# Kernel tuning notes

Hardware: AMD Instinct MI355X
Metric: run time of the kernel (lower is better)

The kernel has to match this reference:

```python
import jax, jax.numpy as jnp
import numpy as np

B, H, S, D = 2, 12, 3456, 32
FEATS_PER_T = 216
WINDOW_LEN = 8
ACT_SIZE = 16
IMG_FEAT_SIZE = 196
DECODER_ONLY = False


def eye_mask(seq_len, feats_per_t, window_len, act_size, img_feat_size, decoder_only=False):
    """Boolean [S, S] mask replicating get_eye_block_mask's memory_mask."""
    idx = jnp.arange(seq_len)
    q_t = (idx // feats_per_t)[:, None]          # [S,1]
    kv_t = (idx // feats_per_t)[None, :]         # [1,S]
    q_m = (idx % feats_per_t)[:, None]
    kv_m = (idx % feats_per_t)[None, :]
    proprio_idx_mod = 2 + 1 + 1
    img_start = feats_per_t - img_feat_size
    joint_start = img_start - act_size

    causal = (q_t >= kv_t) & (q_t - kv_t < window_len)
    is_q_img = q_m >= img_start
    is_kv_img = kv_m >= img_start
    is_q_joint = (q_m >= joint_start) & (q_m < img_start)
    is_kv_joint = (kv_m >= joint_start) & (kv_m < img_start)
    is_kv_proprio = kv_m == proprio_idx_mod

    img_to_img = ~(is_q_img & is_kv_img)
    same_t = q_t == kv_t
    joint_past_joint = ~(is_q_joint & is_kv_joint & ~same_t)
    proprio_past = ~(is_kv_proprio & (kv_t < q_t))
    past_image = ~(is_kv_img & (kv_t < q_t))
    m = causal & img_to_img & joint_past_joint & proprio_past & past_image
    if decoder_only:
        m = m & ~(is_q_img & ~is_kv_img)
    return m


def setup_inputs() -> dict:
    key = jax.random.key(0)
    kq, kk, kv = jax.random.split(key, 3)
    return {
        "q": jax.random.normal(kq, (B, H, S, D), dtype=jnp.float32),
        "k": jax.random.normal(kk, (B, H, S, D), dtype=jnp.float32),
        "v": jax.random.normal(kv, (B, H, S, D), dtype=jnp.float32),
        "feats_per_t": FEATS_PER_T,
        "window_len": WINDOW_LEN,
        "act_size": ACT_SIZE,
        "img_feat_size": IMG_FEAT_SIZE,
    }


def reference(q, k, v, feats_per_t, window_len, act_size, img_feat_size):
    seq_len = q.shape[2]
    mask = eye_mask(seq_len, feats_per_t, window_len, act_size,
                    img_feat_size, DECODER_ONLY)  # [S,S]
    scale = 1.0 / jnp.sqrt(jnp.array(q.shape[-1], q.dtype))
    scores = jnp.einsum("bhqd,bhkd->bhqk", q, k) * scale
    neg = jnp.asarray(jnp.finfo(scores.dtype).min, scores.dtype)
    scores = jnp.where(mask[None, None], scores, neg)
    attn = jax.nn.softmax(scores, axis=-1)
    return jnp.einsum("bhqk,bhkd->bhqd", attn, v)
```

## Files before the change

kernel.cpp:

```cpp
#include <hip/hip_runtime.h>

#define SEQ   3456
#define DH    32
#define FPT   216
#define NT    16
#define IMG0  20
#define SCALE 0.17677669529663687f

#define KPAD 40
#define VPAD 168
#define PPAD 36

typedef __attribute__((ext_vector_type(8))) short bf16x8;
typedef __attribute__((ext_vector_type(4))) float f32x4;

#define MFMA16(a,b,c) __builtin_amdgcn_mfma_f32_16x16x32_bf16(a,b,c,0,0,0)

__device__ __forceinline__ unsigned short bfh(float f) {
    unsigned u = __float_as_uint(f);
    u += 0x7FFFu + ((u >> 16) & 1u);
    return (unsigned short)(u >> 16);
}
__device__ __forceinline__ float bff(unsigned short h) {
    return __uint_as_float((unsigned)h << 16);
}
__device__ __forceinline__ void split8(const float* f, bf16x8& hi, bf16x8& lo) {
    #pragma unroll
    for (int j = 0; j < 8; ++j) {
        unsigned short h = bfh(f[j]);
        hi[j] = (short)h;
        lo[j] = (short)bfh(f[j] - bff(h));
    }
}

__global__ __launch_bounds__(256)
void eye_attn_mfma(const float* __restrict__ q, const float* __restrict__ k,
                   const float* __restrict__ v, float* __restrict__ out) {
    __shared__ __align__(16) unsigned short KsHi[160 * KPAD];
    __shared__ __align__(16) unsigned short KsLo[160 * KPAD];
    __shared__ __align__(16) unsigned short VtHi[DH * VPAD];
    __shared__ __align__(16) unsigned short VtLo[DH * VPAD];
    __shared__ __align__(16) float Pl[4 * 16 * PPAD];

    const int t = blockIdx.x, bh = blockIdx.y, tid = threadIdx.x;
    const size_t base = (size_t)bh * SEQ * DH;
    const int dmax = (t < 7) ? t : 7;
    const int nkeys = IMG0 * (dmax + 1);

    for (int i = tid; i < 160 * 8; i += 256) {
        const int g = i >> 3, c = i & 7;
        float4 kk = make_float4(0.f,0.f,0.f,0.f), vv = make_float4(0.f,0.f,0.f,0.f);
        if (g < nkeys) {
            const int d = g / IMG0, jj = g - d * IMG0;
            const size_t row = base + (size_t)((t - d) * FPT + jj) * DH + c * 4;
            kk = *(const float4*)(k + row);
            vv = *(const float4*)(v + row);
        }
        const float kf[4] = {kk.x, kk.y, kk.z, kk.w};
        const float vf[4] = {vv.x, vv.y, vv.z, vv.w};
        ushort4 khi, klo;
        unsigned short* ah = (unsigned short*)&khi;
        unsigned short* al = (unsigned short*)&klo;
        #pragma unroll
        for (int e = 0; e < 4; ++e) {
            const unsigned short h = bfh(kf[e]);
            ah[e] = h;
            al[e] = bfh(kf[e] - bff(h));
        }
        *(ushort4*)(KsHi + g * KPAD + c * 4) = khi;
        *(ushort4*)(KsLo + g * KPAD + c * 4) = klo;
        #pragma unroll
        for (int e = 0; e < 4; ++e) {
            const unsigned short h = bfh(vf[e]);
            VtHi[(c * 4 + e) * VPAD + g] = h;
            VtLo[(c * 4 + e) * VPAD + g] = bfh(vf[e] - bff(h));
        }
    }
    __syncthreads();

    const int wv = tid >> 6, lane = tid & 63;
    const int col = lane & 15, quad = lane >> 4;

    int mtiles[4]; int mcnt;
    if (wv == 0)      { mtiles[0]=0;  mtiles[1]=2;  mtiles[2]=3;  mtiles[3]=0; mcnt=3; }
    else if (wv == 1) { mtiles[0]=1;  mtiles[1]=4;  mtiles[2]=5;  mtiles[3]=0; mcnt=3; }
    else if (wv == 2) { mtiles[0]=6;  mtiles[1]=7;  mtiles[2]=8;  mtiles[3]=9; mcnt=4; }
    else              { mtiles[0]=10; mtiles[1]=11; mtiles[2]=12; mtiles[3]=13; mcnt=4; }

    bf16x8 bones;
    #pragma unroll
    for (int j = 0; j < 8; ++j) bones[j] = (short)(col == 0 ? 0x3F80 : 0);

    float* myP = Pl + wv * 16 * PPAD;
    const int nkt = (nkeys + 31) >> 5;

    for (int mi = 0; mi < mcnt; ++mi) {
        const int mb = mtiles[mi] * 16;
        bf16x8 qhi, qlo;
        {
            const int qc = min(mb + col, FPT - 1);
            const float* qp = q + base + (size_t)(t * FPT + qc) * DH + quad * 8;
            float qf[8];
            const float4 a0 = *(const float4*)qp;
            const float4 a1 = *(const float4*)(qp + 4);
            qf[0]=a0.x*SCALE; qf[1]=a0.y*SCALE; qf[2]=a0.z*SCALE; qf[3]=a0.w*SCALE;
            qf[4]=a1.x*SCALE; qf[5]=a1.y*SCALE; qf[6]=a1.z*SCALE; qf[7]=a1.w*SCALE;
            split8(qf, qhi, qlo);
        }
        f32x4 oacc0 = {0.f,0.f,0.f,0.f}, oacc1 = {0.f,0.f,0.f,0.f};
        f32x4 lacc = {0.f,0.f,0.f,0.f};

        for (int kt = 0; kt < nkt; ++kt) {
            f32x4 s[2];
            #pragma unroll
            for (int h = 0; h < 2; ++h) {
                const int key = kt * 32 + h * 16 + col;
                const bf16x8 bhi = *(const bf16x8*)(KsHi + key * KPAD + quad * 8);
                const bf16x8 blo = *(const bf16x8*)(KsLo + key * KPAD + quad * 8);
                f32x4 acc = {0.f,0.f,0.f,0.f};
                acc = MFMA16(qhi, bhi, acc);
                acc = MFMA16(qlo, bhi, acc);
                acc = MFMA16(qhi, blo, acc);
                s[h] = acc;
            }
            #pragma unroll
            for (int h = 0; h < 2; ++h) {
                const int g = kt * 32 + h * 16 + col;
                const int d = g / IMG0, jj = g - d * IMG0;
                #pragma unroll
                for (int r = 0; r < 4; ++r) {
                    const int qm = mb + quad * 4 + r;
                    const bool qj = (qm >= 4) && (qm < IMG0);
                    const bool vis = (g < nkeys) && (qm < FPT) &&
                                     ((d == 0) || ((jj != 4) && !(qj && jj >= 4)));
                    const float e = vis ? __expf(s[h][r]) : 0.f;
                    myP[(quad * 4 + r) * PPAD + h * 16 + col] = e;
                }
            }
            bf16x8 phi, plo;
            {
                const float* pr = myP + col * PPAD + quad * 8;
                float pf[8];
                const float4 p0 = *(const float4*)pr;
                const float4 p1 = *(const float4*)(pr + 4);
                pf[0]=p0.x; pf[1]=p0.y; pf[2]=p0.z; pf[3]=p0.w;
                pf[4]=p1.x; pf[5]=p1.y; pf[6]=p1.z; pf[7]=p1.w;
                split8(pf, phi, plo);
            }
            #pragma unroll
            for (int h = 0; h < 2; ++h) {
                const int dim = h * 16 + col;
                const bf16x8 vhi = *(const bf16x8*)(VtHi + dim * VPAD + kt * 32 + quad * 8);
                const bf16x8 vlo = *(const bf16x8*)(VtLo + dim * VPAD + kt * 32 + quad * 8);
                f32x4& oa = h ? oacc1 : oacc0;
                oa = MFMA16(phi, vhi, oa);
                oa = MFMA16(plo, vhi, oa);
                oa = MFMA16(phi, vlo, oa);
            }
            lacc = MFMA16(phi, bones, lacc);
            lacc = MFMA16(plo, bones, lacc);
        }

        if (mi == 0 && wv < 2) {
            for (int kt2 = 0; kt2 < 7; ++kt2) {
                f32x4 s[2];
                #pragma unroll
                for (int h = 0; h < 2; ++h) {
                    const int keyc = min(IMG0 + kt2 * 32 + h * 16 + col, FPT - 1);
                    const float* kp = k + base + (size_t)(t * FPT + keyc) * DH + quad * 8;
                    float kf[8];
                    const float4 a0 = *(const float4*)kp;
                    const float4 a1 = *(const float4*)(kp + 4);
                    kf[0]=a0.x; kf[1]=a0.y; kf[2]=a0.z; kf[3]=a0.w;
                    kf[4]=a1.x; kf[5]=a1.y; kf[6]=a1.z; kf[7]=a1.w;
                    bf16x8 khi, klo;
                    split8(kf, khi, klo);
                    f32x4 acc = {0.f,0.f,0.f,0.f};
                    acc = MFMA16(qhi, khi, acc);
                    acc = MFMA16(qlo, khi, acc);
                    acc = MFMA16(qhi, klo, acc);
                    s[h] = acc;
                }
                #pragma unroll
                for (int h = 0; h < 2; ++h) {
                    const int key = IMG0 + kt2 * 32 + h * 16 + col;
                    #pragma unroll
                    for (int r = 0; r < 4; ++r) {
                        const int qm = mb + quad * 4 + r;
                        const bool vis = (key < FPT) && (qm < IMG0);
                        const float e = vis ? __expf(s[h][r]) : 0.f;
                        myP[(quad * 4 + r) * PPAD + h * 16 + col] = e;
                    }
                }
                bf16x8 phi, plo;
                {
                    const float* pr = myP + col * PPAD + quad * 8;
                    float pf[8];
                    const float4 p0 = *(const float4*)pr;
                    const float4 p1 = *(const float4*)(pr + 4);
                    pf[0]=p0.x; pf[1]=p0.y; pf[2]=p0.z; pf[3]=p0.w;
                    pf[4]=p1.x; pf[5]=p1.y; pf[6]=p1.z; pf[7]=p1.w;
                    split8(pf, phi, plo);
                }
                #pragma unroll
                for (int h = 0; h < 2; ++h) {
                    const int dim = h * 16 + col;
                    float vf[8];
                    #pragma unroll
                    for (int j = 0; j < 8; ++j) {
                        const int ky = min(IMG0 + kt2 * 32 + quad * 8 + j, FPT - 1);
                        vf[j] = v[base + (size_t)(t * FPT + ky) * DH + dim];
                    }
                    bf16x8 vhi, vlo;
                    split8(vf, vhi, vlo);
                    f32x4& oa = h ? oacc1 : oacc0;
                    oa = MFMA16(phi, vhi, oa);
                    oa = MFMA16(plo, vhi, oa);
                    oa = MFMA16(phi, vlo, oa);
                }
                lacc = MFMA16(phi, bones, lacc);
                lacc = MFMA16(plo, bones, lacc);
            }
        }

        #pragma unroll
        for (int r = 0; r < 4; ++r) {
            const float lr = __shfl(lacc[r], lane & 48);
            const float inv = 1.f / lr;
            const int qm = mb + quad * 4 + r;
            if (qm < FPT) {
                float* op = out + base + (size_t)(t * FPT + qm) * DH;
                op[col]      = oacc0[r] * inv;
                op[16 + col] = oacc1[r] * inv;
            }
        }
    }
}

extern "C" void kernel_launch(void* const* d_in, const int* in_sizes, int n_in,
                              void* d_out, int out_size, void* d_ws, size_t ws_size,
                              hipStream_t stream) {
    const float* q = (const float*)d_in[0];
    const float* k = (const float*)d_in[1];
    const float* v = (const float*)d_in[2];
    float* out = (float*)d_out;
    const int BH = in_sizes[0] / (SEQ * DH);
    dim3 grid(NT, BH);
    eye_attn_mfma<<<grid, 256, 0, stream>>>(q, k, v, out);
}
```

Before: 110.3 us.

## Drop bf16 lo-split on P and V, split query tiles across two blocks

The P·V product now uses single bf16 terms for P and V instead of the three-term hi/lo split. This removes VtLo and cuts the PV and row-sum MFMA count to a third. P is stored directly as bf16 in shared memory rather than as float followed by a re-split. Query tiles are also spread over a new grid z-dimension of two, doubling the block count, with each block redoing the K/V staging. The cost is lower accuracy in the probabilities and values, and duplicated shared-memory load work per block.

```diff
diff --git a/kernel.cpp b/kernel.cpp
--- a/kernel.cpp
+++ b/kernel.cpp
@@ -7,9 +7,9 @@
 #define IMG0  20
 #define SCALE 0.17677669529663687f
 
-#define KPAD 40
-#define VPAD 168
-#define PPAD 36
+#define KPAD   40
+#define VPAD   168
+#define PPITCH 40
 
 typedef __attribute__((ext_vector_type(8))) short bf16x8;
 typedef __attribute__((ext_vector_type(4))) float f32x4;
@@ -34,15 +34,15 @@
 }
 
 __global__ __launch_bounds__(256)
-void eye_attn_mfma(const float* __restrict__ q, const float* __restrict__ k,
-                   const float* __restrict__ v, float* __restrict__ out) {
+void eye_attn_mfma2(const float* __restrict__ q, const float* __restrict__ k,
+                    const float* __restrict__ v, float* __restrict__ out) {
     __shared__ __align__(16) unsigned short KsHi[160 * KPAD];
     __shared__ __align__(16) unsigned short KsLo[160 * KPAD];
     __shared__ __align__(16) unsigned short VtHi[DH * VPAD];
-    __shared__ __align__(16) unsigned short VtLo[DH * VPAD];
-    __shared__ __align__(16) float Pl[4 * 16 * PPAD];
-
-    const int t = blockIdx.x, bh = blockIdx.y, tid = threadIdx.x;
+    __shared__ __align__(16) unsigned short Pu[4 * 16 * PPITCH];
+
+    const int t = blockIdx.x, bh = blockIdx.y, half = blockIdx.z;
+    const int tid = threadIdx.x;
     const size_t base = (size_t)bh * SEQ * DH;
     const int dmax = (t < 7) ? t : 7;
     const int nkeys = IMG0 * (dmax + 1);
@@ -70,32 +70,33 @@
         *(ushort4*)(KsHi + g * KPAD + c * 4) = khi;
         *(ushort4*)(KsLo + g * KPAD + c * 4) = klo;
         #pragma unroll
-        for (int e = 0; e < 4; ++e) {
-            const unsigned short h = bfh(vf[e]);
-            VtHi[(c * 4 + e) * VPAD + g] = h;
-            VtLo[(c * 4 + e) * VPAD + g] = bfh(vf[e] - bff(h));
-        }
+        for (int e = 0; e < 4; ++e)
+            VtHi[(c * 4 + e) * VPAD + g] = bfh(vf[e]);
     }
     __syncthreads();
 
     const int wv = tid >> 6, lane = tid & 63;
     const int col = lane & 15, quad = lane >> 4;
 
-    int mtiles[4]; int mcnt;
-    if (wv == 0)      { mtiles[0]=0;  mtiles[1]=2;  mtiles[2]=3;  mtiles[3]=0; mcnt=3; }
-    else if (wv == 1) { mtiles[0]=1;  mtiles[1]=4;  mtiles[2]=5;  mtiles[3]=0; mcnt=3; }
-    else if (wv == 2) { mtiles[0]=6;  mtiles[1]=7;  mtiles[2]=8;  mtiles[3]=9; mcnt=4; }
-    else              { mtiles[0]=10; mtiles[1]=11; mtiles[2]=12; mtiles[3]=13; mcnt=4; }
+    int mt[2]; int mcnt; bool do_img = false;
+    if (half == 0) {
+        if (wv == 0)      { mt[0] = 0; mcnt = 1; do_img = true; }
+        else if (wv == 1) { mt[0] = 1; mcnt = 1; do_img = true; }
+        else if (wv == 2) { mt[0] = 2; mt[1] = 3; mcnt = 2; }
+        else              { mt[0] = 4; mt[1] = 5; mcnt = 2; }
+    } else {
+        mt[0] = 6 + 2 * wv; mt[1] = 7 + 2 * wv; mcnt = 2;
+    }
 
     bf16x8 bones;
     #pragma unroll
     for (int j = 0; j < 8; ++j) bones[j] = (short)(col == 0 ? 0x3F80 : 0);
 
-    float* myP = Pl + wv * 16 * PPAD;
+    unsigned short* myP = Pu + wv * 16 * PPITCH;
     const int nkt = (nkeys + 31) >> 5;
 
     for (int mi = 0; mi < mcnt; ++mi) {
-        const int mb = mtiles[mi] * 16;
+        const int mb = mt[mi] * 16;
         bf16x8 qhi, qlo;
         {
             const int qc = min(mb + col, FPT - 1);
@@ -115,12 +116,12 @@
             #pragma unroll
             for (int h = 0; h < 2; ++h) {
                 const int key = kt * 32 + h * 16 + col;
-                const bf16x8 bhi = *(const bf16x8*)(KsHi + key * KPAD + quad * 8);
-                const bf16x8 blo = *(const bf16x8*)(KsLo + key * KPAD + quad * 8);
+                const bf16x8 khi = *(const bf16x8*)(KsHi + key * KPAD + quad * 8);
+                const bf16x8 klo = *(const bf16x8*)(KsLo + key * KPAD + quad * 8);
                 f32x4 acc = {0.f,0.f,0.f,0.f};
-                acc = MFMA16(qhi, bhi, acc);
-                acc = MFMA16(qlo, bhi, acc);
-                acc = MFMA16(qhi, blo, acc);
+                acc = MFMA16(qhi, khi, acc);
+                acc = MFMA16(qlo, khi, acc);
+                acc = MFMA16(qhi, klo, acc);
                 s[h] = acc;
             }
             #pragma unroll
@@ -134,34 +135,21 @@
                     const bool vis = (g < nkeys) && (qm < FPT) &&
                                      ((d == 0) || ((jj != 4) && !(qj && jj >= 4)));
                     const float e = vis ? __expf(s[h][r]) : 0.f;
-                    myP[(quad * 4 + r) * PPAD + h * 16 + col] = e;
-                }
-            }
-            bf16x8 phi, plo;
-            {
-                const float* pr = myP + col * PPAD + quad * 8;
-                float pf[8];
-                const float4 p0 = *(const float4*)pr;
-                const float4 p1 = *(const float4*)(pr + 4);
-                pf[0]=p0.x; pf[1]=p0.y; pf[2]=p0.z; pf[3]=p0.w;
-                pf[4]=p1.x; pf[5]=p1.y; pf[6]=p1.z; pf[7]=p1.w;
-                split8(pf, phi, plo);
-            }
+                    myP[(quad * 4 + r) * PPITCH + h * 16 + col] = bfh(e);
+                }
+            }
+            const bf16x8 phi = *(const bf16x8*)(myP + col * PPITCH + quad * 8);
             #pragma unroll
             for (int h = 0; h < 2; ++h) {
                 const int dim = h * 16 + col;
                 const bf16x8 vhi = *(const bf16x8*)(VtHi + dim * VPAD + kt * 32 + quad * 8);
-                const bf16x8 vlo = *(const bf16x8*)(VtLo + dim * VPAD + kt * 32 + quad * 8);
                 f32x4& oa = h ? oacc1 : oacc0;
                 oa = MFMA16(phi, vhi, oa);
-                oa = MFMA16(plo, vhi, oa);
-                oa = MFMA16(phi, vlo, oa);
             }
             lacc = MFMA16(phi, bones, lacc);
-            lacc = MFMA16(plo, bones, lacc);
-        }
-
-        if (mi == 0 && wv < 2) {
+        }
+
+        if (mi == 0 && do_img) {
             for (int kt2 = 0; kt2 < 7; ++kt2) {
                 f32x4 s[2];
                 #pragma unroll
@@ -189,19 +177,10 @@
                         const int qm = mb + quad * 4 + r;
                         const bool vis = (key < FPT) && (qm < IMG0);
                         const float e = vis ? __expf(s[h][r]) : 0.f;
-                        myP[(quad * 4 + r) * PPAD + h * 16 + col] = e;
+                        myP[(quad * 4 + r) * PPITCH + h * 16 + col] = bfh(e);
                     }
                 }
-                bf16x8 phi, plo;
-                {
-                    const float* pr = myP + col * PPAD + quad * 8;
-                    float pf[8];
-                    const float4 p0 = *(const float4*)pr;
-                    const float4 p1 = *(const float4*)(pr + 4);
-                    pf[0]=p0.x; pf[1]=p0.y; pf[2]=p0.z; pf[3]=p0.w;
-                    pf[4]=p1.x; pf[5]=p1.y; pf[6]=p1.z; pf[7]=p1.w;
-                    split8(pf, phi, plo);
-                }
+                const bf16x8 phi = *(const bf16x8*)(myP + col * PPITCH + quad * 8);
                 #pragma unroll
                 for (int h = 0; h < 2; ++h) {
                     const int dim = h * 16 + col;
@@ -211,15 +190,13 @@
                         const int ky = min(IMG0 + kt2 * 32 + quad * 8 + j, FPT - 1);
                         vf[j] = v[base + (size_t)(t * FPT + ky) * DH + dim];
                     }
-                    bf16x8 vhi, vlo;
-                    split8(vf, vhi, vlo);
+                    bf16x8 vhi;
+                    #pragma unroll
+                    for (int j = 0; j < 8; ++j) vhi[j] = (short)bfh(vf[j]);
                     f32x4& oa = h ? oacc1 : oacc0;
                     oa = MFMA16(phi, vhi, oa);
-                    oa = MFMA16(plo, vhi, oa);
-                    oa = MFMA16(phi, vlo, oa);
                 }
                 lacc = MFMA16(phi, bones, lacc);
-                lacc = MFMA16(plo, bones, lacc);
             }
         }
 
@@ -245,6 +222,6 @@
     const float* v = (const float*)d_in[2];
     float* out = (float*)d_out;
     const int BH = in_sizes[0] / (SEQ * DH);
-    dim3 grid(NT, BH);
-    eye_attn_mfma<<<grid, 256, 0, stream>>>(q, k, v, out);
-}
+    dim3 grid(NT, BH, 2);
+    eye_attn_mfma2<<<grid, 256, 0, stream>>>(q, k, v, out);
+}
```

Result: faster. 97.72 us (median of 2 runs) (-11.4%).
